# Kernel optimization log

Measured on AMD Instinct MI355X. Metric: run time of the kernel, lower is better.

Reference implementation:

```python
import jax, jax.numpy as jnp
import numpy as np

D_MODEL = 1024
NUM_HEADS = 16
HEAD_DIM = D_MODEL // NUM_HEADS
BATCH = 4
SEQ = 1024


def setup_inputs() -> dict:
    key = jax.random.key(0)
    ks = jax.random.split(key, 11)
    s = 1.0 / np.sqrt(D_MODEL)
    return {
        "query": jax.random.normal(ks[0], (BATCH, SEQ, D_MODEL), jnp.float32),
        "key_": jax.random.normal(ks[1], (BATCH, SEQ, D_MODEL), jnp.float32),
        "value": jax.random.normal(ks[2], (BATCH, SEQ, D_MODEL), jnp.float32),
        "Wq": jax.random.uniform(ks[3], (D_MODEL, D_MODEL), jnp.float32, -s, s),
        "bq": jax.random.uniform(ks[4], (D_MODEL,), jnp.float32, -s, s),
        "Wk": jax.random.uniform(ks[5], (D_MODEL, D_MODEL), jnp.float32, -s, s),
        "bk": jax.random.uniform(ks[6], (D_MODEL,), jnp.float32, -s, s),
        "Wv": jax.random.uniform(ks[7], (D_MODEL, D_MODEL), jnp.float32, -s, s),
        "bv": jax.random.uniform(ks[8], (D_MODEL,), jnp.float32, -s, s),
        "Wo": jax.random.uniform(ks[9], (D_MODEL, D_MODEL), jnp.float32, -s, s),
        "bo": jax.random.uniform(ks[10], (D_MODEL,), jnp.float32, -s, s),
    }


def reference(query, key_, value, Wq, bq, Wk, bk, Wv, bv, Wo, bo):
    B, S, _ = query.shape
    scale = 1.0 / np.sqrt(HEAD_DIM).astype(np.float32)
    # projections, then split heads: [B, H, S, Dh]
    Q = (query @ Wq.T + bq).reshape(B, S, NUM_HEADS, HEAD_DIM).transpose(0, 2, 1, 3)
    K = (key_ @ Wk.T + bk).reshape(B, S, NUM_HEADS, HEAD_DIM).transpose(0, 2, 1, 3)
    V = (value @ Wv.T + bv).reshape(B, S, NUM_HEADS, HEAD_DIM).transpose(0, 2, 1, 3)
    scores = jnp.einsum("bhqd,bhkd->bhqk", Q, K) * scale
    attention = jax.nn.softmax(scores, axis=-1)
    out = jnp.einsum("bhqk,bhkd->bhqd", attention, V)
    out = out.transpose(0, 2, 1, 3).reshape(B, S, D_MODEL)
    return out @ Wo.T + bo, attention
```

## Files before the change

### kernel.cpp

```cpp
#include <hip/hip_runtime.h>
#include <hip/hip_bf16.h>

#define NH 16
#define S 1024
#define DH 64
#define DM 1024
#define MTOK 4096

typedef __attribute__((ext_vector_type(8))) short bf16x8;
typedef __attribute__((ext_vector_type(4))) float f32x4;
typedef __attribute__((ext_vector_type(16))) float f32x16;
typedef __attribute__((ext_vector_type(8))) unsigned short u16x8;
typedef __attribute__((ext_vector_type(4))) unsigned short u16x4;

__device__ inline unsigned short f2bf(float x) {
  __hip_bfloat16 h = __float2bfloat16(x);
  return __builtin_bit_cast(unsigned short, h);
}

__device__ inline unsigned cvt_pk_bf16(float lo, float hi_) {
  unsigned r;
  asm("v_cvt_pk_bf16_f32 %0, %1, %2" : "=v"(r) : "v"(lo), "v"(hi_));
  return r;
}

__device__ inline void gload16(const void* g, void* lds) {
  __builtin_amdgcn_global_load_lds((const __attribute__((address_space(1))) void*)g,
                                   (__attribute__((address_space(3))) void*)lds, 16, 0, 0);
}

__global__ __launch_bounds__(256) void cvt_all(
    const float* __restrict__ q, const float* __restrict__ k, const float* __restrict__ v,
    const float* __restrict__ wq, const float* __restrict__ wk,
    const float* __restrict__ wv, const float* __restrict__ wo,
    unsigned short* __restrict__ xq, unsigned short* __restrict__ xk,
    unsigned short* __restrict__ xv, unsigned short* __restrict__ wqb,
    unsigned short* __restrict__ wkb, unsigned short* __restrict__ wvb,
    unsigned short* __restrict__ wob) {
  const int bid = blockIdx.x;
  const float* src;
  unsigned short* dst;
  int lb;
  if (bid < 6144) {
    const int r = bid >> 11;
    lb = bid & 2047;
    src = (r == 0) ? q : ((r == 1) ? k : v);
    dst = (r == 0) ? xq : ((r == 1) ? xk : xv);
  } else {
    const int r = (bid - 6144) >> 9;
    lb = (bid - 6144) & 511;
    src = (r == 0) ? wq : ((r == 1) ? wk : ((r == 2) ? wv : wo));
    dst = (r == 0) ? wqb : ((r == 1) ? wkb : ((r == 2) ? wvb : wob));
  }
  const int i = lb * 256 + threadIdx.x;
  const float4* s4 = (const float4*)(src + (size_t)i * 8);
  float4 v0 = s4[0], v1 = s4[1];
  u16x8 o;
  o[0] = f2bf(v0.x); o[1] = f2bf(v0.y); o[2] = f2bf(v0.z); o[3] = f2bf(v0.w);
  o[4] = f2bf(v1.x); o[5] = f2bf(v1.y); o[6] = f2bf(v1.z); o[7] = f2bf(v1.w);
  *(u16x8*)(dst + (size_t)i * 8) = o;
}

__device__ inline void gemm_core(const unsigned short* __restrict__ X,
                                 const unsigned short* __restrict__ W,
                                 unsigned short* As, unsigned short* Bs,
                                 int m0, int n0, f32x4 acc[2][4]) {
  const int t = threadIdx.x, l = t & 63, w = t >> 6;
  const int i4 = l >> 2, c8 = (l & 3) * 8;
  const int wr = w >> 1, wc = w & 1, cl = l & 15, kg = l >> 4;

  const unsigned short* ga  = X + (size_t)(m0 + w * 16 + i4) * DM + c8;
  const unsigned short* gb0 = W + (size_t)(n0 + w * 32 + i4) * DM + c8;
  const unsigned short* gb1 = W + (size_t)(n0 + w * 32 + 16 + i4) * DM + c8;
  char* lA  = (char*)As + w * 1024;
  char* lB0 = (char*)Bs + w * 2048;
  char* lB1 = (char*)Bs + w * 2048 + 1024;

  for (int kt = 0; kt < DM; kt += 32) {
    __syncthreads();
    gload16(ga + kt, lA);
    gload16(gb0 + kt, lB0);
    gload16(gb1 + kt, lB1);
    __syncthreads();
    bf16x8 a[2], b[4];
#pragma unroll
    for (int i = 0; i < 2; ++i)
      a[i] = *(const bf16x8*)&As[(wr * 32 + i * 16 + cl) * 32 + kg * 8];
#pragma unroll
    for (int j = 0; j < 4; ++j)
      b[j] = *(const bf16x8*)&Bs[(wc * 64 + j * 16 + cl) * 32 + kg * 8];
#pragma unroll
    for (int i = 0; i < 2; ++i)
#pragma unroll
      for (int j = 0; j < 4; ++j)
        acc[i][j] = __builtin_amdgcn_mfma_f32_16x16x32_bf16(a[i], b[j], acc[i][j], 0, 0, 0);
  }
}

__global__ __launch_bounds__(256) void proj_gemm(
    const unsigned short* __restrict__ X0, const unsigned short* __restrict__ X1,
    const unsigned short* __restrict__ X2, const unsigned short* __restrict__ W0,
    const unsigned short* __restrict__ W1, const unsigned short* __restrict__ W2,
    const float* __restrict__ b0, const float* __restrict__ b1, const float* __restrict__ b2,
    unsigned short* __restrict__ Y0, unsigned short* __restrict__ Y1,
    unsigned short* __restrict__ Y2) {
  __shared__ unsigned short As[64 * 32];
  __shared__ unsigned short Bs[128 * 32];
  const int z = blockIdx.z;
  const unsigned short* X = (z == 0) ? X0 : ((z == 1) ? X1 : X2);
  const unsigned short* W = (z == 0) ? W0 : ((z == 1) ? W1 : W2);
  const float* bias = (z == 0) ? b0 : ((z == 1) ? b1 : b2);
  const int m0 = blockIdx.y * 64, n0 = blockIdx.x * 128;

  f32x4 acc[2][4] = {};
  gemm_core(X, W, As, Bs, m0, n0, acc);

  const int l = threadIdx.x & 63, w = threadIdx.x >> 6;
  const int wr = w >> 1, wc = w & 1, cl = l & 15, kg = l >> 4;
#pragma unroll
  for (int i = 0; i < 2; ++i) {
#pragma unroll
    for (int j = 0; j < 4; ++j) {
      const int gn = n0 + wc * 64 + j * 16 + cl;
      const float bv = bias[gn];
      const int h_ = gn >> 6, d_ = gn & 63;
#pragma unroll
      for (int r = 0; r < 4; ++r) {
        const int gm = m0 + wr * 32 + i * 16 + kg * 4 + r;
        const int b_ = gm >> 10, s_ = gm & 1023;
        const float val = acc[i][j][r] + bv;
        if (z == 0) {
          Y0[((size_t)(b_ * NH + h_) * S + s_) * DH + d_] = f2bf(val);
        } else if (z == 1) {
          Y1[((size_t)(b_ * NH + h_) * S + s_) * DH + d_] = f2bf(val * 0.125f);
        } else {
          Y2[((size_t)(b_ * NH + h_) * DH + d_) * S + s_] = f2bf(val);
        }
      }
    }
  }
}

__global__ __launch_bounds__(256) void out_gemm(const unsigned short* __restrict__ X,
                                                const unsigned short* __restrict__ W,
                                                const float* __restrict__ bias,
                                                float* __restrict__ Y) {
  __shared__ unsigned short As[64 * 32];
  __shared__ unsigned short Bs[128 * 32];
  const int m0 = blockIdx.y * 64, n0 = blockIdx.x * 128;
  f32x4 acc[2][4] = {};
  gemm_core(X, W, As, Bs, m0, n0, acc);
  const int l = threadIdx.x & 63, w = threadIdx.x >> 6;
  const int wr = w >> 1, wc = w & 1, cl = l & 15, kg = l >> 4;
#pragma unroll
  for (int i = 0; i < 2; ++i) {
#pragma unroll
    for (int j = 0; j < 4; ++j) {
      const int gn = n0 + wc * 64 + j * 16 + cl;
      const float bv = bias[gn];
#pragma unroll
      for (int r = 0; r < 4; ++r) {
        const int gm = m0 + wr * 32 + i * 16 + kg * 4 + r;
        Y[(size_t)gm * DM + gn] = acc[i][j][r] + bv;
      }
    }
  }
}

__global__ __launch_bounds__(256) void attn_mfma(const unsigned short* __restrict__ Qh,
                                                 const unsigned short* __restrict__ Kh,
                                                 const unsigned short* __restrict__ Vt,
                                                 float* __restrict__ attn,
                                                 unsigned short* __restrict__ OutH) {
  __shared__ float sums[4][32];
  __shared__ float Olds[4][32][68];
  const int t = threadIdx.x, l = t & 63, w = t >> 6;
  const int lq = l & 31, hi = l >> 5;
  const int bh = blockIdx.y;
  const int q0 = blockIdx.x * 32;

  const unsigned short* qp = Qh + ((size_t)bh * S + q0 + lq) * DH + hi * 8;
  bf16x8 qf0 = *(const bf16x8*)(qp);
  bf16x8 qf1 = *(const bf16x8*)(qp + 16);
  bf16x8 qf2 = *(const bf16x8*)(qp + 32);
  bf16x8 qf3 = *(const bf16x8*)(qp + 48);

  const unsigned short* kb = Kh + (size_t)bh * S * DH + (size_t)w * 256 * DH;
  const unsigned short* vb = Vt + (size_t)bh * DH * S + w * 256;

  float sum = 0.f;
  for (int kt = 0; kt < 8; ++kt) {
    const unsigned short* kp = kb + (size_t)(kt * 32 + lq) * DH + hi * 8;
    f32x16 acc = {};
    acc = __builtin_amdgcn_mfma_f32_32x32x16_bf16(*(const bf16x8*)(kp),      qf0, acc, 0, 0, 0);
    acc = __builtin_amdgcn_mfma_f32_32x32x16_bf16(*(const bf16x8*)(kp + 16), qf1, acc, 0, 0, 0);
    acc = __builtin_amdgcn_mfma_f32_32x32x16_bf16(*(const bf16x8*)(kp + 32), qf2, acc, 0, 0, 0);
    acc = __builtin_amdgcn_mfma_f32_32x32x16_bf16(*(const bf16x8*)(kp + 48), qf3, acc, 0, 0, 0);
    float ls = 0.f;
#pragma unroll
    for (int r = 0; r < 16; ++r) ls += __expf(acc[r]);
    sum += ls;
  }
  sum += __shfl_xor(sum, 32);
  if (l < 32) sums[w][lq] = sum;
  __syncthreads();
  const float inv = 1.0f / (sums[0][lq] + sums[1][lq] + sums[2][lq] + sums[3][lq]);

  f32x16 o0 = {}, o1 = {};
  float* ab = attn + ((size_t)bh << 20) + ((size_t)(q0 + lq) << 10) + w * 256;

  for (int kt = 0; kt < 8; ++kt) {
    const unsigned short* kp2 = kb + (size_t)(kt * 32 + lq) * DH + hi * 8;
    f32x16 acc = {};
    acc = __builtin_amdgcn_mfma_f32_32x32x16_bf16(*(const bf16x8*)(kp2),      qf0, acc, 0, 0, 0);
    acc = __builtin_amdgcn_mfma_f32_32x32x16_bf16(*(const bf16x8*)(kp2 + 16), qf1, acc, 0, 0, 0);
    acc = __builtin_amdgcn_mfma_f32_32x32x16_bf16(*(const bf16x8*)(kp2 + 32), qf2, acc, 0, 0, 0);
    acc = __builtin_amdgcn_mfma_f32_32x32x16_bf16(*(const bf16x8*)(kp2 + 48), qf3, acc, 0, 0, 0);
    float p[16];
#pragma unroll
    for (int r = 0; r < 16; ++r) p[r] = __expf(acc[r]) * inv;

#pragma unroll
    for (int g = 0; g < 4; ++g) {
      f32x4 pv = {p[4 * g], p[4 * g + 1], p[4 * g + 2], p[4 * g + 3]};
      *(f32x4*)(ab + kt * 32 + 8 * g + 4 * hi) = pv;
    }

    unsigned wds0 = cvt_pk_bf16(p[0], p[1]),   wds1 = cvt_pk_bf16(p[2], p[3]);
    unsigned wds2 = cvt_pk_bf16(p[4], p[5]),   wds3 = cvt_pk_bf16(p[6], p[7]);
    unsigned wds4 = cvt_pk_bf16(p[8], p[9]),   wds5 = cvt_pk_bf16(p[10], p[11]);
    unsigned wds6 = cvt_pk_bf16(p[12], p[13]), wds7 = cvt_pk_bf16(p[14], p[15]);
    unsigned x0 = __shfl_xor((int)wds0, 32), x1 = __shfl_xor((int)wds1, 32);
    unsigned x2 = __shfl_xor((int)wds2, 32), x3 = __shfl_xor((int)wds3, 32);
    unsigned x4 = __shfl_xor((int)wds4, 32), x5 = __shfl_xor((int)wds5, 32);
    unsigned x6 = __shfl_xor((int)wds6, 32), x7 = __shfl_xor((int)wds7, 32);
    union UU { unsigned u[4]; bf16x8 v; } f0, f1;
    f0.u[0] = hi ? x2 : wds0;  f0.u[1] = hi ? x3 : wds1;
    f0.u[2] = hi ? wds2 : x0;  f0.u[3] = hi ? wds3 : x1;
    f1.u[0] = hi ? x6 : wds4;  f1.u[1] = hi ? x7 : wds5;
    f1.u[2] = hi ? wds6 : x4;  f1.u[3] = hi ? wds7 : x5;

    {
      const unsigned short* vp = vb + (size_t)(lq)*S + kt * 32 + hi * 8;
      bf16x8 v0 = *(const bf16x8*)vp;
      bf16x8 v1 = *(const bf16x8*)(vp + 16);
      o0 = __builtin_amdgcn_mfma_f32_32x32x16_bf16(v0, f0.v, o0, 0, 0, 0);
      o0 = __builtin_amdgcn_mfma_f32_32x32x16_bf16(v1, f1.v, o0, 0, 0, 0);
    }
    {
      const unsigned short* vp = vb + (size_t)(32 + lq) * S + kt * 32 + hi * 8;
      bf16x8 v0 = *(const bf16x8*)vp;
      bf16x8 v1 = *(const bf16x8*)(vp + 16);
      o1 = __builtin_amdgcn_mfma_f32_32x32x16_bf16(v0, f0.v, o1, 0, 0, 0);
      o1 = __builtin_amdgcn_mfma_f32_32x32x16_bf16(v1, f1.v, o1, 0, 0, 0);
    }
  }

#pragma unroll
  for (int g = 0; g < 4; ++g) {
    f32x4 a = {o0[4 * g], o0[4 * g + 1], o0[4 * g + 2], o0[4 * g + 3]};
    *(f32x4*)&Olds[w][lq][8 * g + 4 * hi] = a;
    f32x4 b2 = {o1[4 * g], o1[4 * g + 1], o1[4 * g + 2], o1[4 * g + 3]};
    *(f32x4*)&Olds[w][lq][32 + 8 * g + 4 * hi] = b2;
  }
  __syncthreads();

  const int b_ = bh >> 4, h_ = bh & 15;
  const int qq = t >> 3, d0 = (t & 7) * 8;
  u16x8 ov;
#pragma unroll
  for (int i = 0; i < 8; ++i) {
    const float s = Olds[0][qq][d0 + i] + Olds[1][qq][d0 + i] +
                    Olds[2][qq][d0 + i] + Olds[3][qq][d0 + i];
    ov[i] = f2bf(s);
  }
  *(u16x8*)&OutH[((size_t)(b_ * S + q0 + qq)) * DM + h_ * DH + d0] = ov;
}

extern "C" void kernel_launch(void* const* d_in, const int* in_sizes, int n_in,
                              void* d_out, int out_size, void* d_ws, size_t ws_size,
                              hipStream_t stream) {
  const float* query = (const float*)d_in[0];
  const float* key_  = (const float*)d_in[1];
  const float* value = (const float*)d_in[2];
  const float* Wq = (const float*)d_in[3];
  const float* bq = (const float*)d_in[4];
  const float* Wk = (const float*)d_in[5];
  const float* bk = (const float*)d_in[6];
  const float* Wv = (const float*)d_in[7];
  const float* bv = (const float*)d_in[8];
  const float* Wo = (const float*)d_in[9];
  const float* bo = (const float*)d_in[10];

  float* out0 = (float*)d_out;
  float* attn = out0 + (size_t)MTOK * DM;

  const size_t M1 = 1u << 20;
  unsigned short* wsu = (unsigned short*)d_ws;
  unsigned short* Xq  = wsu;
  unsigned short* Xk  = wsu + 4 * M1;
  unsigned short* Xv  = wsu + 8 * M1;
  unsigned short* Wqb = wsu + 12 * M1;
  unsigned short* Wkb = wsu + 13 * M1;
  unsigned short* Wvb = wsu + 14 * M1;
  unsigned short* Wob = wsu + 15 * M1;
  unsigned short* Qh  = wsu + 16 * M1;
  unsigned short* Kh  = wsu + 20 * M1;
  unsigned short* Vt  = wsu + 24 * M1;
  unsigned short* OutH= wsu + 28 * M1;

  dim3 tB(256);
  hipLaunchKernelGGL(cvt_all, dim3(8192), tB, 0, stream, query, key_, value, Wq, Wk, Wv, Wo,
                     Xq, Xk, Xv, Wqb, Wkb, Wvb, Wob);

  hipLaunchKernelGGL(proj_gemm, dim3(8, 64, 3), tB, 0, stream,
                     Xq, Xk, Xv, Wqb, Wkb, Wvb, bq, bk, bv, Qh, Kh, Vt);

  hipLaunchKernelGGL(attn_mfma, dim3(32, 64), tB, 0, stream, Qh, Kh, Vt, attn, OutH);

  hipLaunchKernelGGL(out_gemm, dim3(8, 64), tB, 0, stream, OutH, Wob, bo, out0);
}
```

Baseline: 242.6 us.

## Enlarge GEMM tiles to 128x128 and cache exp scores across 8-wave attention

The projection and output GEMMs move from 64x128 to 128x128 block tiles, with each wave computing a 64x64 sub-tile, to raise operand reuse and halve the grid. The attention kernel moves to 512 threads (8 waves, 128 keys each) and keeps exp(scores) packed as bf16 in registers, so the second QK^T pass and its exp are no longer recomputed. Normalisation is applied to the PV accumulators at the end, and the cross-wave reduction uses a padded transposed LDS layout. In exchange, the attention probabilities written out are now rounded through bf16, which lowers their precision, and register pressure rises in both kernels.

```diff
diff --git a/kernel.cpp b/kernel.cpp
--- a/kernel.cpp
+++ b/kernel.cpp
@@ -61,39 +61,43 @@
   *(u16x8*)(dst + (size_t)i * 8) = o;
 }
 
-__device__ inline void gemm_core(const unsigned short* __restrict__ X,
-                                 const unsigned short* __restrict__ W,
-                                 unsigned short* As, unsigned short* Bs,
-                                 int m0, int n0, f32x4 acc[2][4]) {
+__device__ inline void gemm_core128(const unsigned short* __restrict__ X,
+                                    const unsigned short* __restrict__ W,
+                                    unsigned short* As, unsigned short* Bs,
+                                    int m0, int n0, f32x4 acc[4][4]) {
   const int t = threadIdx.x, l = t & 63, w = t >> 6;
-  const int i4 = l >> 2, c8 = (l & 3) * 8;
   const int wr = w >> 1, wc = w & 1, cl = l & 15, kg = l >> 4;
-
-  const unsigned short* ga  = X + (size_t)(m0 + w * 16 + i4) * DM + c8;
-  const unsigned short* gb0 = W + (size_t)(n0 + w * 32 + i4) * DM + c8;
-  const unsigned short* gb1 = W + (size_t)(n0 + w * 32 + 16 + i4) * DM + c8;
-  char* lA  = (char*)As + w * 1024;
-  char* lB0 = (char*)Bs + w * 2048;
-  char* lB1 = (char*)Bs + w * 2048 + 1024;
+  const int row0 = w * 16 + (l >> 2);
+  const int kcol = (l & 3) * 8;
+
+  const unsigned short* ga0 = X + (size_t)(m0 + row0) * DM + kcol;
+  const unsigned short* ga1 = ga0 + (size_t)64 * DM;
+  const unsigned short* gb0 = W + (size_t)(n0 + row0) * DM + kcol;
+  const unsigned short* gb1 = gb0 + (size_t)64 * DM;
+  char* lA0 = (char*)As + w * 1024;
+  char* lA1 = (char*)As + w * 1024 + 4096;
+  char* lB0 = (char*)Bs + w * 1024;
+  char* lB1 = (char*)Bs + w * 1024 + 4096;
 
   for (int kt = 0; kt < DM; kt += 32) {
     __syncthreads();
-    gload16(ga + kt, lA);
+    gload16(ga0 + kt, lA0);
+    gload16(ga1 + kt, lA1);
     gload16(gb0 + kt, lB0);
     gload16(gb1 + kt, lB1);
     __syncthreads();
-    bf16x8 a[2], b[4];
-#pragma unroll
-    for (int i = 0; i < 2; ++i)
-      a[i] = *(const bf16x8*)&As[(wr * 32 + i * 16 + cl) * 32 + kg * 8];
-#pragma unroll
-    for (int j = 0; j < 4; ++j)
-      b[j] = *(const bf16x8*)&Bs[(wc * 64 + j * 16 + cl) * 32 + kg * 8];
-#pragma unroll
-    for (int i = 0; i < 2; ++i)
-#pragma unroll
-      for (int j = 0; j < 4; ++j)
-        acc[i][j] = __builtin_amdgcn_mfma_f32_16x16x32_bf16(a[i], b[j], acc[i][j], 0, 0, 0);
+    bf16x8 a[4], b[4];
+#pragma unroll
+    for (int m = 0; m < 4; ++m)
+      a[m] = *(const bf16x8*)&As[(wr * 64 + m * 16 + cl) * 32 + kg * 8];
+#pragma unroll
+    for (int n = 0; n < 4; ++n)
+      b[n] = *(const bf16x8*)&Bs[(wc * 64 + n * 16 + cl) * 32 + kg * 8];
+#pragma unroll
+    for (int m = 0; m < 4; ++m)
+#pragma unroll
+      for (int n = 0; n < 4; ++n)
+        acc[m][n] = __builtin_amdgcn_mfma_f32_16x16x32_bf16(a[m], b[n], acc[m][n], 0, 0, 0);
   }
 }
 
@@ -104,21 +108,21 @@
     const float* __restrict__ b0, const float* __restrict__ b1, const float* __restrict__ b2,
     unsigned short* __restrict__ Y0, unsigned short* __restrict__ Y1,
     unsigned short* __restrict__ Y2) {
-  __shared__ unsigned short As[64 * 32];
+  __shared__ unsigned short As[128 * 32];
   __shared__ unsigned short Bs[128 * 32];
   const int z = blockIdx.z;
   const unsigned short* X = (z == 0) ? X0 : ((z == 1) ? X1 : X2);
   const unsigned short* W = (z == 0) ? W0 : ((z == 1) ? W1 : W2);
   const float* bias = (z == 0) ? b0 : ((z == 1) ? b1 : b2);
-  const int m0 = blockIdx.y * 64, n0 = blockIdx.x * 128;
-
-  f32x4 acc[2][4] = {};
-  gemm_core(X, W, As, Bs, m0, n0, acc);
+  const int m0 = blockIdx.y * 128, n0 = blockIdx.x * 128;
+
+  f32x4 acc[4][4] = {};
+  gemm_core128(X, W, As, Bs, m0, n0, acc);
 
   const int l = threadIdx.x & 63, w = threadIdx.x >> 6;
   const int wr = w >> 1, wc = w & 1, cl = l & 15, kg = l >> 4;
 #pragma unroll
-  for (int i = 0; i < 2; ++i) {
+  for (int i = 0; i < 4; ++i) {
 #pragma unroll
     for (int j = 0; j < 4; ++j) {
       const int gn = n0 + wc * 64 + j * 16 + cl;
@@ -126,7 +130,7 @@
       const int h_ = gn >> 6, d_ = gn & 63;
 #pragma unroll
       for (int r = 0; r < 4; ++r) {
-        const int gm = m0 + wr * 32 + i * 16 + kg * 4 + r;
+        const int gm = m0 + wr * 64 + i * 16 + kg * 4 + r;
         const int b_ = gm >> 10, s_ = gm & 1023;
         const float val = acc[i][j][r] + bv;
         if (z == 0) {
@@ -145,95 +149,101 @@
                                                 const unsigned short* __restrict__ W,
                                                 const float* __restrict__ bias,
                                                 float* __restrict__ Y) {
-  __shared__ unsigned short As[64 * 32];
+  __shared__ unsigned short As[128 * 32];
   __shared__ unsigned short Bs[128 * 32];
-  const int m0 = blockIdx.y * 64, n0 = blockIdx.x * 128;
-  f32x4 acc[2][4] = {};
-  gemm_core(X, W, As, Bs, m0, n0, acc);
+  const int m0 = blockIdx.y * 128, n0 = blockIdx.x * 128;
+  f32x4 acc[4][4] = {};
+  gemm_core128(X, W, As, Bs, m0, n0, acc);
   const int l = threadIdx.x & 63, w = threadIdx.x >> 6;
   const int wr = w >> 1, wc = w & 1, cl = l & 15, kg = l >> 4;
 #pragma unroll
-  for (int i = 0; i < 2; ++i) {
+  for (int i = 0; i < 4; ++i) {
 #pragma unroll
     for (int j = 0; j < 4; ++j) {
       const int gn = n0 + wc * 64 + j * 16 + cl;
       const float bv = bias[gn];
 #pragma unroll
       for (int r = 0; r < 4; ++r) {
-        const int gm = m0 + wr * 32 + i * 16 + kg * 4 + r;
+        const int gm = m0 + wr * 64 + i * 16 + kg * 4 + r;
         Y[(size_t)gm * DM + gn] = acc[i][j][r] + bv;
       }
     }
   }
 }
 
-__global__ __launch_bounds__(256) void attn_mfma(const unsigned short* __restrict__ Qh,
-                                                 const unsigned short* __restrict__ Kh,
-                                                 const unsigned short* __restrict__ Vt,
-                                                 float* __restrict__ attn,
-                                                 unsigned short* __restrict__ OutH) {
-  __shared__ float sums[4][32];
-  __shared__ float Olds[4][32][68];
+__global__ __launch_bounds__(512, 4) void attn_mfma(const unsigned short* __restrict__ Qh,
+                                                    const unsigned short* __restrict__ Kh,
+                                                    const unsigned short* __restrict__ Vt,
+                                                    float* __restrict__ attn,
+                                                    unsigned short* __restrict__ OutH) {
+  __shared__ float sums[8][32];
+  __shared__ float Olds[8 * 64 * 33];
   const int t = threadIdx.x, l = t & 63, w = t >> 6;
   const int lq = l & 31, hi = l >> 5;
   const int bh = blockIdx.y;
   const int q0 = blockIdx.x * 32;
 
-  const unsigned short* qp = Qh + ((size_t)bh * S + q0 + lq) * DH + hi * 8;
-  bf16x8 qf0 = *(const bf16x8*)(qp);
-  bf16x8 qf1 = *(const bf16x8*)(qp + 16);
-  bf16x8 qf2 = *(const bf16x8*)(qp + 32);
-  bf16x8 qf3 = *(const bf16x8*)(qp + 48);
-
-  const unsigned short* kb = Kh + (size_t)bh * S * DH + (size_t)w * 256 * DH;
-  const unsigned short* vb = Vt + (size_t)bh * DH * S + w * 256;
-
+  const unsigned short* kb = Kh + (size_t)bh * S * DH;
+  const unsigned short* vb = Vt + (size_t)bh * DH * S;
+
+  unsigned e_pk[4][8];
   float sum = 0.f;
-  for (int kt = 0; kt < 8; ++kt) {
-    const unsigned short* kp = kb + (size_t)(kt * 32 + lq) * DH + hi * 8;
-    f32x16 acc = {};
-    acc = __builtin_amdgcn_mfma_f32_32x32x16_bf16(*(const bf16x8*)(kp),      qf0, acc, 0, 0, 0);
-    acc = __builtin_amdgcn_mfma_f32_32x32x16_bf16(*(const bf16x8*)(kp + 16), qf1, acc, 0, 0, 0);
-    acc = __builtin_amdgcn_mfma_f32_32x32x16_bf16(*(const bf16x8*)(kp + 32), qf2, acc, 0, 0, 0);
-    acc = __builtin_amdgcn_mfma_f32_32x32x16_bf16(*(const bf16x8*)(kp + 48), qf3, acc, 0, 0, 0);
-    float ls = 0.f;
-#pragma unroll
-    for (int r = 0; r < 16; ++r) ls += __expf(acc[r]);
-    sum += ls;
+
+  {
+    const unsigned short* qp = Qh + ((size_t)bh * S + q0 + lq) * DH + hi * 8;
+    bf16x8 qf0 = *(const bf16x8*)(qp);
+    bf16x8 qf1 = *(const bf16x8*)(qp + 16);
+    bf16x8 qf2 = *(const bf16x8*)(qp + 32);
+    bf16x8 qf3 = *(const bf16x8*)(qp + 48);
+#pragma unroll
+    for (int kt = 0; kt < 4; ++kt) {
+      const unsigned short* kp = kb + (size_t)(w * 128 + kt * 32 + lq) * DH + hi * 8;
+      f32x16 acc = {};
+      acc = __builtin_amdgcn_mfma_f32_32x32x16_bf16(*(const bf16x8*)(kp),      qf0, acc, 0, 0, 0);
+      acc = __builtin_amdgcn_mfma_f32_32x32x16_bf16(*(const bf16x8*)(kp + 16), qf1, acc, 0, 0, 0);
+      acc = __builtin_amdgcn_mfma_f32_32x32x16_bf16(*(const bf16x8*)(kp + 32), qf2, acc, 0, 0, 0);
+      acc = __builtin_amdgcn_mfma_f32_32x32x16_bf16(*(const bf16x8*)(kp + 48), qf3, acc, 0, 0, 0);
+      float e[16];
+#pragma unroll
+      for (int r = 0; r < 16; ++r) e[r] = __expf(acc[r]);
+#pragma unroll
+      for (int r = 0; r < 16; ++r) sum += e[r];
+#pragma unroll
+      for (int j = 0; j < 8; ++j) e_pk[kt][j] = cvt_pk_bf16(e[2 * j], e[2 * j + 1]);
+    }
   }
   sum += __shfl_xor(sum, 32);
   if (l < 32) sums[w][lq] = sum;
   __syncthreads();
-  const float inv = 1.0f / (sums[0][lq] + sums[1][lq] + sums[2][lq] + sums[3][lq]);
+  float tot = 0.f;
+#pragma unroll
+  for (int p = 0; p < 8; ++p) tot += sums[p][lq];
+  const float inv = 1.0f / tot;
 
   f32x16 o0 = {}, o1 = {};
-  float* ab = attn + ((size_t)bh << 20) + ((size_t)(q0 + lq) << 10) + w * 256;
-
-  for (int kt = 0; kt < 8; ++kt) {
-    const unsigned short* kp2 = kb + (size_t)(kt * 32 + lq) * DH + hi * 8;
-    f32x16 acc = {};
-    acc = __builtin_amdgcn_mfma_f32_32x32x16_bf16(*(const bf16x8*)(kp2),      qf0, acc, 0, 0, 0);
-    acc = __builtin_amdgcn_mfma_f32_32x32x16_bf16(*(const bf16x8*)(kp2 + 16), qf1, acc, 0, 0, 0);
-    acc = __builtin_amdgcn_mfma_f32_32x32x16_bf16(*(const bf16x8*)(kp2 + 32), qf2, acc, 0, 0, 0);
-    acc = __builtin_amdgcn_mfma_f32_32x32x16_bf16(*(const bf16x8*)(kp2 + 48), qf3, acc, 0, 0, 0);
-    float p[16];
-#pragma unroll
-    for (int r = 0; r < 16; ++r) p[r] = __expf(acc[r]) * inv;
-
+  float* ab = attn + ((size_t)bh << 20) + ((size_t)(q0 + lq) << 10) + w * 128;
+
+#pragma unroll
+  for (int kt = 0; kt < 4; ++kt) {
 #pragma unroll
     for (int g = 0; g < 4; ++g) {
-      f32x4 pv = {p[4 * g], p[4 * g + 1], p[4 * g + 2], p[4 * g + 3]};
+      const unsigned pk0 = e_pk[kt][2 * g], pk1 = e_pk[kt][2 * g + 1];
+      f32x4 pv;
+      pv[0] = __builtin_bit_cast(float, pk0 << 16) * inv;
+      pv[1] = __builtin_bit_cast(float, pk0 & 0xffff0000u) * inv;
+      pv[2] = __builtin_bit_cast(float, pk1 << 16) * inv;
+      pv[3] = __builtin_bit_cast(float, pk1 & 0xffff0000u) * inv;
       *(f32x4*)(ab + kt * 32 + 8 * g + 4 * hi) = pv;
     }
 
-    unsigned wds0 = cvt_pk_bf16(p[0], p[1]),   wds1 = cvt_pk_bf16(p[2], p[3]);
-    unsigned wds2 = cvt_pk_bf16(p[4], p[5]),   wds3 = cvt_pk_bf16(p[6], p[7]);
-    unsigned wds4 = cvt_pk_bf16(p[8], p[9]),   wds5 = cvt_pk_bf16(p[10], p[11]);
-    unsigned wds6 = cvt_pk_bf16(p[12], p[13]), wds7 = cvt_pk_bf16(p[14], p[15]);
-    unsigned x0 = __shfl_xor((int)wds0, 32), x1 = __shfl_xor((int)wds1, 32);
-    unsigned x2 = __shfl_xor((int)wds2, 32), x3 = __shfl_xor((int)wds3, 32);
-    unsigned x4 = __shfl_xor((int)wds4, 32), x5 = __shfl_xor((int)wds5, 32);
-    unsigned x6 = __shfl_xor((int)wds6, 32), x7 = __shfl_xor((int)wds7, 32);
+    const unsigned wds0 = e_pk[kt][0], wds1 = e_pk[kt][1];
+    const unsigned wds2 = e_pk[kt][2], wds3 = e_pk[kt][3];
+    const unsigned wds4 = e_pk[kt][4], wds5 = e_pk[kt][5];
+    const unsigned wds6 = e_pk[kt][6], wds7 = e_pk[kt][7];
+    const unsigned x0 = __shfl_xor((int)wds0, 32), x1 = __shfl_xor((int)wds1, 32);
+    const unsigned x2 = __shfl_xor((int)wds2, 32), x3 = __shfl_xor((int)wds3, 32);
+    const unsigned x4 = __shfl_xor((int)wds4, 32), x5 = __shfl_xor((int)wds5, 32);
+    const unsigned x6 = __shfl_xor((int)wds6, 32), x7 = __shfl_xor((int)wds7, 32);
     union UU { unsigned u[4]; bf16x8 v; } f0, f1;
     f0.u[0] = hi ? x2 : wds0;  f0.u[1] = hi ? x3 : wds1;
     f0.u[2] = hi ? wds2 : x0;  f0.u[3] = hi ? wds3 : x1;
@@ -241,14 +251,14 @@
     f1.u[2] = hi ? wds6 : x4;  f1.u[3] = hi ? wds7 : x5;
 
     {
-      const unsigned short* vp = vb + (size_t)(lq)*S + kt * 32 + hi * 8;
+      const unsigned short* vp = vb + (size_t)(lq)*S + w * 128 + kt * 32 + hi * 8;
       bf16x8 v0 = *(const bf16x8*)vp;
       bf16x8 v1 = *(const bf16x8*)(vp + 16);
       o0 = __builtin_amdgcn_mfma_f32_32x32x16_bf16(v0, f0.v, o0, 0, 0, 0);
       o0 = __builtin_amdgcn_mfma_f32_32x32x16_bf16(v1, f1.v, o0, 0, 0, 0);
     }
     {
-      const unsigned short* vp = vb + (size_t)(32 + lq) * S + kt * 32 + hi * 8;
+      const unsigned short* vp = vb + (size_t)(32 + lq) * S + w * 128 + kt * 32 + hi * 8;
       bf16x8 v0 = *(const bf16x8*)vp;
       bf16x8 v1 = *(const bf16x8*)(vp + 16);
       o1 = __builtin_amdgcn_mfma_f32_32x32x16_bf16(v0, f0.v, o1, 0, 0, 0);
@@ -257,24 +267,31 @@
   }
 
 #pragma unroll
+  for (int r = 0; r < 16; ++r) { o0[r] *= inv; o1[r] *= inv; }
+#pragma unroll
   for (int g = 0; g < 4; ++g) {
-    f32x4 a = {o0[4 * g], o0[4 * g + 1], o0[4 * g + 2], o0[4 * g + 3]};
-    *(f32x4*)&Olds[w][lq][8 * g + 4 * hi] = a;
-    f32x4 b2 = {o1[4 * g], o1[4 * g + 1], o1[4 * g + 2], o1[4 * g + 3]};
-    *(f32x4*)&Olds[w][lq][32 + 8 * g + 4 * hi] = b2;
+#pragma unroll
+    for (int r = 0; r < 4; ++r) {
+      const int d = 8 * g + 4 * hi + r;
+      Olds[w * 2112 + d * 33 + lq] = o0[4 * g + r];
+      Olds[w * 2112 + (32 + d) * 33 + lq] = o1[4 * g + r];
+    }
   }
   __syncthreads();
 
-  const int b_ = bh >> 4, h_ = bh & 15;
-  const int qq = t >> 3, d0 = (t & 7) * 8;
-  u16x8 ov;
-#pragma unroll
-  for (int i = 0; i < 8; ++i) {
-    const float s = Olds[0][qq][d0 + i] + Olds[1][qq][d0 + i] +
-                    Olds[2][qq][d0 + i] + Olds[3][qq][d0 + i];
-    ov[i] = f2bf(s);
-  }
-  *(u16x8*)&OutH[((size_t)(b_ * S + q0 + qq)) * DM + h_ * DH + d0] = ov;
+  if (t < 256) {
+    const int qq = t >> 3, d0 = (t & 7) * 8;
+    const int b_ = bh >> 4, h_ = bh & 15;
+    u16x8 ov;
+#pragma unroll
+    for (int i = 0; i < 8; ++i) {
+      float s = 0.f;
+#pragma unroll
+      for (int p = 0; p < 8; ++p) s += Olds[p * 2112 + (d0 + i) * 33 + qq];
+      ov[i] = f2bf(s);
+    }
+    *(u16x8*)&OutH[((size_t)(b_ * S + q0 + qq)) * DM + h_ * DH + d0] = ov;
+  }
 }
 
 extern "C" void kernel_launch(void* const* d_in, const int* in_sizes, int n_in,
@@ -313,10 +330,10 @@
   hipLaunchKernelGGL(cvt_all, dim3(8192), tB, 0, stream, query, key_, value, Wq, Wk, Wv, Wo,
                      Xq, Xk, Xv, Wqb, Wkb, Wvb, Wob);
 
-  hipLaunchKernelGGL(proj_gemm, dim3(8, 64, 3), tB, 0, stream,
+  hipLaunchKernelGGL(proj_gemm, dim3(8, 32, 3), tB, 0, stream,
                      Xq, Xk, Xv, Wqb, Wkb, Wvb, bq, bk, bv, Qh, Kh, Vt);
 
-  hipLaunchKernelGGL(attn_mfma, dim3(32, 64), tB, 0, stream, Qh, Kh, Vt, attn, OutH);
-
-  hipLaunchKernelGGL(out_gemm, dim3(8, 64), tB, 0, stream, OutH, Wob, bo, out0);
-}
+  hipLaunchKernelGGL(attn_mfma, dim3(32, 64), dim3(512), 0, stream, Qh, Kh, Vt, attn, OutH);
+
+  hipLaunchKernelGGL(out_gemm, dim3(8, 32), tB, 0, stream, OutH, Wob, bo, out0);
+}
```

After: 212.8 us. 1.14x faster.
